# Performance work log

Hardware: AMD Instinct MI355X
Metric: run time of the kernel (lower is better)

Reference implementation:

```python
import jax, jax.numpy as jnp
import numpy as np

NEG_BIG = -9e15  # matches torch's -9000000000000000.0 mask value
LRELU_ALPHA = 0.2


def setup_inputs() -> dict:
    key = jax.random.key(0)
    ks = jax.random.split(key, 6)
    B, N, Fin, Fout = 2, 4096, 64, 64
    x = jax.random.normal(ks[0], (B, N, Fin), jnp.float32)
    pos = jax.random.normal(ks[1], (B, N, 3), jnp.float32)
    # xavier-ish scaled params
    W = jax.random.normal(ks[2], (Fin, Fout), jnp.float32) * (1.0 / np.sqrt(Fin))
    a = jax.random.normal(ks[3], (2 * Fout, 1), jnp.float32) * (1.0 / np.sqrt(2 * Fout))
    Wp = jax.random.normal(ks[4], (3, Fout), jnp.float32) * (1.0 / np.sqrt(3))
    bp = jnp.zeros((Fout,), jnp.float32)
    return {"x": x, "pos": pos, "W": W, "a": a, "Wp": Wp, "bp": bp, "k": 20}


def reference(x, pos, W, a, Wp, bp, k):
    B, N, _ = x.shape
    Fout = W.shape[1]
    Wh = x @ W  # [B,N,Fout]

    # Dynamic kNN graph (adj=None path): squared-distance ranking == cdist ranking
    sq = jnp.sum(pos * pos, axis=-1)  # [B,N]
    d2 = sq[:, :, None] + sq[:, None, :] - 2.0 * jnp.einsum('bnd,bmd->bnm', pos, pos)
    _, idx = jax.lax.top_k(-d2, k + 1)  # smallest k+1 distances
    idx = idx[:, :, 1:]  # drop self
    adj = jnp.zeros((B, N, N), x.dtype).at[
        jnp.arange(B)[:, None, None], jnp.arange(N)[None, :, None], idx
    ].set(1.0)

    # e[b,i,j] = leakyrelu(a1.Wh_i + a2.Wh_j); decompose instead of O(N^2*2F) concat
    f1 = Wh @ a[:Fout]  # [B,N,1]
    f2 = Wh @ a[Fout:]  # [B,N,1]
    e = f1 + jnp.swapaxes(f2, 1, 2)  # [B,N,N]
    e = jnp.where(e > 0, e, LRELU_ALPHA * e)

    e = jnp.where(adj > 0, e, NEG_BIG)
    attn = jax.nn.softmax(e, axis=2)  # dropout is identity in eval mode

    h = jnp.einsum('bnm,bmf->bnf', attn, Wh) + jax.nn.relu(pos @ Wp + bp)
    return jax.nn.elu(h)  # concat=True path
```

## Files before the change

### kernel.cpp

```cpp
#include <hip/hip_runtime.h>
#include <cfloat>

#define NB 4096
#define FD 64
#define QPB 8
#define LRELU_ALPHA 0.2f
#define CCAP 96

__device__ __forceinline__ float rfl(float v) {
    return __int_as_float(__builtin_amdgcn_readfirstlane(__float_as_int(v)));
}

__global__ __launch_bounds__(256) void prep_kernel(
    const float* __restrict__ x, const float* __restrict__ pos,
    const float* __restrict__ W, const float* __restrict__ a,
    float* __restrict__ Wh, float* __restrict__ f1, float* __restrict__ f2,
    float4* __restrict__ pq)
{
    const int tid = threadIdx.x;
    if (blockIdx.x >= 512) {
        const int i = (blockIdx.x - 512) * 256 + tid;
        const float px = pos[i * 3 + 0];
        const float py = pos[i * 3 + 1];
        const float pz = pos[i * 3 + 2];
        pq[i] = make_float4(px, py, pz, 0.5f * fmaf(pz, pz, fmaf(py, py, px * px)));
        return;
    }
    __shared__ float sW[FD * FD];
    #pragma unroll
    for (int t = 0; t < 16; ++t) sW[tid + t * 256] = W[tid + t * 256];
    __syncthreads();
    const int lane = tid & 63, wave = tid >> 6;
    const float a1v = a[lane], a2v = a[FD + lane];
    const int rbase = blockIdx.x * 16 + wave * 4;
    #pragma unroll
    for (int j = 0; j < 4; j += 2) {
        const int r0 = rbase + j, r1 = rbase + j + 1;
        const float xv0 = x[((size_t)r0 << 6) + lane];
        const float xv1 = x[((size_t)r1 << 6) + lane];
        float acc0 = 0.f, acc1 = 0.f;
        #pragma unroll
        for (int i = 0; i < FD; ++i) {
            const float wv = sW[i * FD + lane];
            acc0 = fmaf(__shfl(xv0, i, 64), wv, acc0);
            acc1 = fmaf(__shfl(xv1, i, 64), wv, acc1);
        }
        Wh[((size_t)r0 << 6) + lane] = acc0;
        Wh[((size_t)r1 << 6) + lane] = acc1;
        float s10 = acc0 * a1v, s20 = acc0 * a2v;
        float s11 = acc1 * a1v, s21 = acc1 * a2v;
        #pragma unroll
        for (int off = 32; off > 0; off >>= 1) {
            s10 += __shfl_down(s10, off, 64);
            s20 += __shfl_down(s20, off, 64);
            s11 += __shfl_down(s11, off, 64);
            s21 += __shfl_down(s21, off, 64);
        }
        if (lane == 0) { f1[r0] = s10; f2[r0] = s20; f1[r1] = s11; f2[r1] = s21; }
    }
}

__global__ __launch_bounds__(256, 8) void gat_fused(
    const float* __restrict__ pos, const float4* __restrict__ pq,
    const float* __restrict__ Wh,
    const float* __restrict__ f1, const float* __restrict__ f2,
    const float* __restrict__ Wp, const float* __restrict__ bp,
    const int* __restrict__ kptr, float* __restrict__ out)
{
    __shared__ union Pool {
        float tmin[QPB * 256];
        struct {
            unsigned long long pkbuf[QPB][CCAP];
            int cidx[QPB][CCAP];
        } s;
    } pool;
    __shared__ float4 sq[QPB];
    __shared__ float sT[QPB];
    __shared__ unsigned int cnt[QPB];
    __shared__ int idx21[QPB][24];

    const int tid = threadIdx.x;
    const int lane = tid & 63, wave = tid >> 6;
    const int qbase = blockIdx.x * QPB;
    const int b = qbase >> 12;
    const float* posb = pos + (size_t)b * NB * 3;
    const float4* pq4 = pq + ((size_t)b << 12);
    const int k = *kptr;

    if (tid < QPB) {
        const int nq = (qbase + tid) & (NB - 1);
        const float ax = posb[nq * 3 + 0], ay = posb[nq * 3 + 1], az = posb[nq * 3 + 2];
        const float sr = __fadd_rn(__fadd_rn(__fmul_rn(ax, ax), __fmul_rn(ay, ay)),
                                   __fmul_rn(az, az));
        sq[tid] = make_float4(ax, ay, az, sr);
        cnt[tid] = 0;
    }
    if (lane < 24) {
        idx21[2 * wave][lane]     = (qbase + 2 * wave) & (NB - 1);
        idx21[2 * wave + 1][lane] = (qbase + 2 * wave + 1) & (NB - 1);
    }
    __syncthreads();

    float qx[QPB], qy[QPB], qz[QPB];
    #pragma unroll
    for (int i = 0; i < QPB; ++i) {
        const int nq = (qbase + i) & (NB - 1);
        qx[i] = rfl(posb[nq * 3 + 0]);
        qy[i] = rfl(posb[nq * 3 + 1]);
        qz[i] = rfl(posb[nq * 3 + 2]);
    }

    float mn[QPB];
    #pragma unroll
    for (int i = 0; i < QPB; ++i) mn[i] = FLT_MAX;
    #pragma unroll 4
    for (int t = 0; t < 16; ++t) {
        const float4 p = pq4[t * 256 + tid];
        #pragma unroll
        for (int i = 0; i < QPB; ++i) {
            const float d = p.w - fmaf(qx[i], p.x, fmaf(qy[i], p.y, qz[i] * p.z));
            mn[i] = fminf(mn[i], d);
        }
    }
    #pragma unroll
    for (int i = 0; i < QPB; ++i) pool.tmin[i * 256 + tid] = mn[i];
    __syncthreads();

    #pragma unroll
    for (int qi = 0; qi < 2; ++qi) {
        const int q = 2 * wave + qi;
        float v = fminf(fminf(pool.tmin[q * 256 + lane],
                              pool.tmin[q * 256 + 64 + lane]),
                        fminf(pool.tmin[q * 256 + 128 + lane],
                              pool.tmin[q * 256 + 192 + lane]));
        #pragma unroll
        for (int kk2 = 2; kk2 <= 64; kk2 <<= 1) {
            #pragma unroll
            for (int j = kk2 >> 1; j > 0; j >>= 1) {
                const float o = __shfl_xor(v, j, 64);
                const bool keepMin = (((lane & j) == 0) == ((lane & kk2) == 0));
                v = keepMin ? fminf(v, o) : fmaxf(v, o);
            }
        }
        const float Tq = __shfl(v, k, 64);
        if (lane == 0) sT[q] = Tq;
    }
    __syncthreads();

    float Ts[QPB];
    #pragma unroll
    for (int i = 0; i < QPB; ++i)
        Ts[i] = sT[i] + 1e-2f + 1e-3f * fabsf(sT[i]);

    #pragma unroll 2
    for (int t = 0; t < 16; ++t) {
        const int m = t * 256 + tid;
        const float4 p = pq4[m];
        #pragma unroll
        for (int i = 0; i < QPB; ++i) {
            const float d = p.w - fmaf(qx[i], p.x, fmaf(qy[i], p.y, qz[i] * p.z));
            if (d <= Ts[i]) {
                const unsigned int pp = atomicAdd(&cnt[i], 1u);
                if (pp < CCAP) pool.s.cidx[i][pp] = m;
            }
        }
    }
    __syncthreads();

    #pragma unroll
    for (int qi = 0; qi < 2; ++qi) {
        const int q = 2 * wave + qi;
        const float4 qq = sq[q];
        const int cn0 = (int)cnt[q];
        const int cn = cn0 < CCAP ? cn0 : CCAP;
        for (int e = lane; e < cn; e += 64) {
            const int m = pool.s.cidx[q][e];
            const float px = posb[m * 3 + 0];
            const float py = posb[m * 3 + 1];
            const float pz = posb[m * 3 + 2];
            const float sqm = __fadd_rn(__fadd_rn(__fmul_rn(px, px), __fmul_rn(py, py)),
                                        __fmul_rn(pz, pz));
            const float dot = __fadd_rn(__fadd_rn(__fmul_rn(qq.x, px), __fmul_rn(qq.y, py)),
                                        __fmul_rn(qq.z, pz));
            const float d2 = __fsub_rn(__fadd_rn(qq.w, sqm), __fmul_rn(2.0f, dot));
            const unsigned int u = __float_as_uint(d2);
            const unsigned int kk = u ^ ((unsigned int)((int)u >> 31) | 0x80000000u);
            pool.s.pkbuf[q][e] = ((unsigned long long)kk << 12) | (unsigned int)m;
        }
        for (int e = lane; e < cn; e += 64) {
            const unsigned long long xv = pool.s.pkbuf[q][e];
            int r = 0;
            for (int j = 0; j < cn; ++j) r += (pool.s.pkbuf[q][j] < xv);
            if (r <= k) idx21[q][r] = (int)(xv & 0xFFFu);
        }

        const int row = qbase + q;
        const bool valid = (lane >= 1 && lane <= k);
        const int nbr = valid ? idx21[q][lane] : 0;
        const float f1v = f1[row];
        float e = -FLT_MAX;
        if (valid) {
            e = f1v + f2[(b << 12) + nbr];
            e = e > 0.f ? e : LRELU_ALPHA * e;
        }
        float mx = e;
        #pragma unroll
        for (int off = 32; off > 0; off >>= 1) mx = fmaxf(mx, __shfl_xor(mx, off, 64));
        const float ex = valid ? __expf(e - mx) : 0.f;
        float Z = ex;
        #pragma unroll
        for (int off = 32; off > 0; off >>= 1) Z += __shfl_xor(Z, off, 64);
        const float attn = ex / Z;

        const float* whb = Wh + (((size_t)b << 12) << 6);
        float h = 0.f;
        #pragma unroll 4
        for (int t = 1; t <= k; ++t) {
            const int nb_ = __shfl(nbr, t, 64);
            const float s = __shfl(attn, t, 64);
            h = fmaf(s, whb[((size_t)nb_ << 6) + lane], h);
        }

        const float pv = fmaf(qq.x, Wp[0 * FD + lane],
                         fmaf(qq.y, Wp[1 * FD + lane],
                         fmaf(qq.z, Wp[2 * FD + lane], bp[lane])));
        h += pv > 0.f ? pv : 0.f;
        out[((size_t)row << 6) + lane] = h > 0.f ? h : expm1f(h);
    }
}

extern "C" void kernel_launch(void* const* d_in, const int* in_sizes, int n_in,
                              void* d_out, int out_size, void* d_ws, size_t ws_size,
                              hipStream_t stream) {
    const float* x   = (const float*)d_in[0];
    const float* pos = (const float*)d_in[1];
    const float* W   = (const float*)d_in[2];
    const float* a   = (const float*)d_in[3];
    const float* Wp  = (const float*)d_in[4];
    const float* bp  = (const float*)d_in[5];
    const int*   kp  = (const int*)d_in[6];

    float* ws = (float*)d_ws;
    float*  Wh = ws;
    float*  f1 = Wh + 524288;
    float*  f2 = f1 + 8192;
    float4* pq = (float4*)(f2 + 8192);
    float*  out = (float*)d_out;

    prep_kernel<<<544, 256, 0, stream>>>(x, pos, W, a, Wh, f1, f2, pq);
    gat_fused<<<(NB * 2) / QPB, 256, 0, stream>>>(pos, pq, Wh, f1, f2, Wp, bp, kp, out);
}
```

Before: 110.0 us.

## Use 512-thread blocks so each wave handles one query, with shuffle-based min reduction

The fused kernel now launches 512 threads, or 8 waves, per block. Each wave owns a single query row, where before each of 4 waves looped over two queries. The per-thread point sweep halves to 8 points per thread, and the 64-bucket minimum used for the kNN threshold is now built with intra-wave xor shuffles over groups of 8 lanes. This replaces a larger shared-memory table and its cross-thread loads. The aim is to parallelise the serial per-query selection, softmax and aggregation tail and to cut shared-memory traffic, at the cost of larger blocks and possible register or occupancy pressure.

```diff
diff --git a/kernel.cpp b/kernel.cpp
--- a/kernel.cpp
+++ b/kernel.cpp
@@ -3,6 +3,8 @@
 
 #define NB 4096
 #define FD 64
+#define NT 512
+#define EPT 8
 #define QPB 8
 #define LRELU_ALPHA 0.2f
 #define CCAP 96
@@ -60,7 +62,7 @@
     }
 }
 
-__global__ __launch_bounds__(256, 8) void gat_fused(
+__global__ __launch_bounds__(NT, 8) void gat_fused(
     const float* __restrict__ pos, const float4* __restrict__ pq,
     const float* __restrict__ Wh,
     const float* __restrict__ f1, const float* __restrict__ f2,
@@ -68,7 +70,7 @@
     const int* __restrict__ kptr, float* __restrict__ out)
 {
     __shared__ union Pool {
-        float tmin[QPB * 256];
+        float tmin[QPB][64];
         struct {
             unsigned long long pkbuf[QPB][CCAP];
             int cidx[QPB][CCAP];
@@ -95,10 +97,7 @@
         sq[tid] = make_float4(ax, ay, az, sr);
         cnt[tid] = 0;
     }
-    if (lane < 24) {
-        idx21[2 * wave][lane]     = (qbase + 2 * wave) & (NB - 1);
-        idx21[2 * wave + 1][lane] = (qbase + 2 * wave + 1) & (NB - 1);
-    }
+    if (lane < 24) idx21[wave][lane] = (qbase + wave) & (NB - 1);
     __syncthreads();
 
     float qx[QPB], qy[QPB], qz[QPB];
@@ -114,8 +113,8 @@
     #pragma unroll
     for (int i = 0; i < QPB; ++i) mn[i] = FLT_MAX;
     #pragma unroll 4
-    for (int t = 0; t < 16; ++t) {
-        const float4 p = pq4[t * 256 + tid];
+    for (int t = 0; t < EPT; ++t) {
+        const float4 p = pq4[t * NT + tid];
         #pragma unroll
         for (int i = 0; i < QPB; ++i) {
             const float d = p.w - fmaf(qx[i], p.x, fmaf(qy[i], p.y, qz[i] * p.z));
@@ -123,16 +122,17 @@
         }
     }
     #pragma unroll
-    for (int i = 0; i < QPB; ++i) pool.tmin[i * 256 + tid] = mn[i];
-    __syncthreads();
-
-    #pragma unroll
-    for (int qi = 0; qi < 2; ++qi) {
-        const int q = 2 * wave + qi;
-        float v = fminf(fminf(pool.tmin[q * 256 + lane],
-                              pool.tmin[q * 256 + 64 + lane]),
-                        fminf(pool.tmin[q * 256 + 128 + lane],
-                              pool.tmin[q * 256 + 192 + lane]));
+    for (int i = 0; i < QPB; ++i) {
+        float v = mn[i];
+        v = fminf(v, __shfl_xor(v, 1, 64));
+        v = fminf(v, __shfl_xor(v, 2, 64));
+        v = fminf(v, __shfl_xor(v, 4, 64));
+        if ((lane & 7) == 0) pool.tmin[i][wave * 8 + (lane >> 3)] = v;
+    }
+    __syncthreads();
+
+    {
+        float v = pool.tmin[wave][lane];
         #pragma unroll
         for (int kk2 = 2; kk2 <= 64; kk2 <<= 1) {
             #pragma unroll
@@ -143,7 +143,7 @@
             }
         }
         const float Tq = __shfl(v, k, 64);
-        if (lane == 0) sT[q] = Tq;
+        if (lane == 0) sT[wave] = Tq;
     }
     __syncthreads();
 
@@ -153,8 +153,8 @@
         Ts[i] = sT[i] + 1e-2f + 1e-3f * fabsf(sT[i]);
 
     #pragma unroll 2
-    for (int t = 0; t < 16; ++t) {
-        const int m = t * 256 + tid;
+    for (int t = 0; t < EPT; ++t) {
+        const int m = t * NT + tid;
         const float4 p = pq4[m];
         #pragma unroll
         for (int i = 0; i < QPB; ++i) {
@@ -167,66 +167,63 @@
     }
     __syncthreads();
 
-    #pragma unroll
-    for (int qi = 0; qi < 2; ++qi) {
-        const int q = 2 * wave + qi;
-        const float4 qq = sq[q];
-        const int cn0 = (int)cnt[q];
-        const int cn = cn0 < CCAP ? cn0 : CCAP;
-        for (int e = lane; e < cn; e += 64) {
-            const int m = pool.s.cidx[q][e];
-            const float px = posb[m * 3 + 0];
-            const float py = posb[m * 3 + 1];
-            const float pz = posb[m * 3 + 2];
-            const float sqm = __fadd_rn(__fadd_rn(__fmul_rn(px, px), __fmul_rn(py, py)),
-                                        __fmul_rn(pz, pz));
-            const float dot = __fadd_rn(__fadd_rn(__fmul_rn(qq.x, px), __fmul_rn(qq.y, py)),
-                                        __fmul_rn(qq.z, pz));
-            const float d2 = __fsub_rn(__fadd_rn(qq.w, sqm), __fmul_rn(2.0f, dot));
-            const unsigned int u = __float_as_uint(d2);
-            const unsigned int kk = u ^ ((unsigned int)((int)u >> 31) | 0x80000000u);
-            pool.s.pkbuf[q][e] = ((unsigned long long)kk << 12) | (unsigned int)m;
-        }
-        for (int e = lane; e < cn; e += 64) {
-            const unsigned long long xv = pool.s.pkbuf[q][e];
-            int r = 0;
-            for (int j = 0; j < cn; ++j) r += (pool.s.pkbuf[q][j] < xv);
-            if (r <= k) idx21[q][r] = (int)(xv & 0xFFFu);
-        }
-
-        const int row = qbase + q;
-        const bool valid = (lane >= 1 && lane <= k);
-        const int nbr = valid ? idx21[q][lane] : 0;
-        const float f1v = f1[row];
-        float e = -FLT_MAX;
-        if (valid) {
-            e = f1v + f2[(b << 12) + nbr];
-            e = e > 0.f ? e : LRELU_ALPHA * e;
-        }
-        float mx = e;
-        #pragma unroll
-        for (int off = 32; off > 0; off >>= 1) mx = fmaxf(mx, __shfl_xor(mx, off, 64));
-        const float ex = valid ? __expf(e - mx) : 0.f;
-        float Z = ex;
-        #pragma unroll
-        for (int off = 32; off > 0; off >>= 1) Z += __shfl_xor(Z, off, 64);
-        const float attn = ex / Z;
-
-        const float* whb = Wh + (((size_t)b << 12) << 6);
-        float h = 0.f;
-        #pragma unroll 4
-        for (int t = 1; t <= k; ++t) {
-            const int nb_ = __shfl(nbr, t, 64);
-            const float s = __shfl(attn, t, 64);
-            h = fmaf(s, whb[((size_t)nb_ << 6) + lane], h);
-        }
-
-        const float pv = fmaf(qq.x, Wp[0 * FD + lane],
-                         fmaf(qq.y, Wp[1 * FD + lane],
-                         fmaf(qq.z, Wp[2 * FD + lane], bp[lane])));
-        h += pv > 0.f ? pv : 0.f;
-        out[((size_t)row << 6) + lane] = h > 0.f ? h : expm1f(h);
-    }
+    const int q = wave;
+    const float4 qq = sq[q];
+    const int cn0 = (int)cnt[q];
+    const int cn = cn0 < CCAP ? cn0 : CCAP;
+    for (int e = lane; e < cn; e += 64) {
+        const int m = pool.s.cidx[q][e];
+        const float px = posb[m * 3 + 0];
+        const float py = posb[m * 3 + 1];
+        const float pz = posb[m * 3 + 2];
+        const float sqm = __fadd_rn(__fadd_rn(__fmul_rn(px, px), __fmul_rn(py, py)),
+                                    __fmul_rn(pz, pz));
+        const float dot = __fadd_rn(__fadd_rn(__fmul_rn(qq.x, px), __fmul_rn(qq.y, py)),
+                                    __fmul_rn(qq.z, pz));
+        const float d2 = __fsub_rn(__fadd_rn(qq.w, sqm), __fmul_rn(2.0f, dot));
+        const unsigned int u = __float_as_uint(d2);
+        const unsigned int kk = u ^ ((unsigned int)((int)u >> 31) | 0x80000000u);
+        pool.s.pkbuf[q][e] = ((unsigned long long)kk << 12) | (unsigned int)m;
+    }
+    for (int e = lane; e < cn; e += 64) {
+        const unsigned long long xv = pool.s.pkbuf[q][e];
+        int r = 0;
+        for (int j = 0; j < cn; ++j) r += (pool.s.pkbuf[q][j] < xv);
+        if (r <= k) idx21[q][r] = (int)(xv & 0xFFFu);
+    }
+
+    const int row = qbase + q;
+    const bool valid = (lane >= 1 && lane <= k);
+    const int nbr = valid ? idx21[q][lane] : 0;
+    const float f1v = f1[row];
+    float e = -FLT_MAX;
+    if (valid) {
+        e = f1v + f2[(b << 12) + nbr];
+        e = e > 0.f ? e : LRELU_ALPHA * e;
+    }
+    float mx = e;
+    #pragma unroll
+    for (int off = 32; off > 0; off >>= 1) mx = fmaxf(mx, __shfl_xor(mx, off, 64));
+    const float ex = valid ? __expf(e - mx) : 0.f;
+    float Z = ex;
+    #pragma unroll
+    for (int off = 32; off > 0; off >>= 1) Z += __shfl_xor(Z, off, 64);
+    const float attn = ex / Z;
+
+    const float* whb = Wh + (((size_t)b << 12) << 6);
+    float h = 0.f;
+    #pragma unroll 4
+    for (int t = 1; t <= k; ++t) {
+        const int nb_ = __shfl(nbr, t, 64);
+        const float s = __shfl(attn, t, 64);
+        h = fmaf(s, whb[((size_t)nb_ << 6) + lane], h);
+    }
+
+    const float pv = fmaf(qq.x, Wp[0 * FD + lane],
+                     fmaf(qq.y, Wp[1 * FD + lane],
+                     fmaf(qq.z, Wp[2 * FD + lane], bp[lane])));
+    h += pv > 0.f ? pv : 0.f;
+    out[((size_t)row << 6) + lane] = h > 0.f ? h : expm1f(h);
 }
 
 extern "C" void kernel_launch(void* const* d_in, const int* in_sizes, int n_in,
@@ -248,5 +245,5 @@
     float*  out = (float*)d_out;
 
     prep_kernel<<<544, 256, 0, stream>>>(x, pos, W, a, Wh, f1, f2, pq);
-    gat_fused<<<(NB * 2) / QPB, 256, 0, stream>>>(pos, pq, Wh, f1, f2, Wp, bp, kp, out);
-}
+    gat_fused<<<(NB * 2) / QPB, NT, 0, stream>>>(pos, pq, Wh, f1, f2, Wp, bp, kp, out);
+}
```

After: 102.3 us. 7.0% less time.
